# Optimization experiments

Hardware: AMD Instinct MI355X
Metric: run time of the kernel (lower is better)

Reference implementation:

```python
import jax, jax.numpy as jnp
import numpy as np

EPS_NORM = 1e-12   # torch F.normalize eps
EPS_COND = 1e-10   # conductance denominator eps (matches source)


def _metrics(rep, b):
    # rep: (N, D) float, b: (N,) int 0/1 boundaries
    N = rep.shape[0]
    S = rep @ rep.T                                   # (N, N) similarity
    # F.normalize(sim, p=2, dim=-1): L2-normalize each row
    S = S / jnp.maximum(jnp.linalg.norm(S, axis=-1, keepdims=True), EPS_NORM)
    comm = jnp.cumsum(b)                              # (N,) community ids in [0, N]
    total = S.sum()
    deg = S.sum(axis=1)                               # row sums
    # modularity: sum over same-community (i, j) of S_ij - deg_i*deg_j/total, then /total
    same = comm[:, None] == comm[None, :]
    mod = jnp.sum(jnp.where(same, S - deg[:, None] * deg[None, :] / total, 0.0)) / total
    # conductance via segment sums over community ids (num_segments fixed = N+1)
    C = N + 1
    A = jax.ops.segment_sum(S, comm, num_segments=C)          # (C, N): sum over rows i in comm c
    B2 = jax.ops.segment_sum(A.T, comm, num_segments=C)      # (C_j, C_i)
    within = jnp.diagonal(B2)                                 # within-community edge weight
    row_tot = A.sum(axis=1)                                   # total weight incident to comm c
    between = row_tot - within
    counts = jax.ops.segment_sum(jnp.ones((N,), dtype=S.dtype), comm, num_segments=C)
    nonempty = counts > 0
    cond_terms = jnp.where(nonempty, between / (2.0 * within + between + EPS_COND), 0.0)
    n_comms = jnp.maximum(nonempty.sum(), 1).astype(S.dtype)
    cond = cond_terms.sum() / n_comms
    return mod, cond


def setup_inputs() -> dict:
    key = jax.random.key(0)
    k1, k2 = jax.random.split(key)
    representations = jax.random.normal(k1, (8, 2048, 512), dtype=jnp.float32)
    boundaries = jax.random.randint(k2, (8, 2048), 0, 2, dtype=jnp.int32)
    return {"representations": representations, "boundaries": boundaries}


def reference(representations, boundaries):
    mod, cond = jax.vmap(_metrics)(representations, boundaries)
    # (2, B): row 0 = modularity per batch, row 1 = conductance per batch
    return jnp.stack([mod, cond], axis=0)
```

## Files before the change

### kernel.cpp

```cpp
#include <hip/hip_runtime.h>
#include <hip/hip_bf16.h>

constexpr int BATCH = 8;
constexpr int N = 2048;
constexpr int D = 512;

using short8 = __attribute__((ext_vector_type(8))) short;
using half8 = __attribute__((ext_vector_type(8))) _Float16;
using floatx4 = __attribute__((ext_vector_type(4))) float;

struct f8 { float4 a, b; };
__device__ __forceinline__ f8 load8(const float* p) {
    f8 r; r.a = *(const float4*)p; r.b = *(const float4*)(p + 4); return r;
}
__device__ __forceinline__ void cvt_split(const f8& v, short8& h, short8& l) {
    const float* f = (const float*)&v;
#pragma unroll
    for (int e = 0; e < 8; ++e) {
        _Float16 hh = (_Float16)f[e];
        float r = f[e] - (float)hh;
        _Float16 ll = (_Float16)r;
        h[e] = __builtin_bit_cast(short, hh);
        l[e] = __builtin_bit_cast(short, ll);
    }
}

__global__ __launch_bounds__(256) void scan_kernel(const int* __restrict__ b,
                                                   int* __restrict__ comm,
                                                   float* __restrict__ stats ) {
    int batch = blockIdx.x;
    int t = threadIdx.x;

    {
        int idx = batch * 256 + t;
#pragma unroll
        for (int u = 0; u < 24; ++u) stats[idx + u * 2048] = 0.0f;
    }

    const int* bb = b + batch * N;
    int* cc = comm + batch * N;
    int vals[8];
    int s = 0;
#pragma unroll
    for (int u = 0; u < 8; ++u) { vals[u] = bb[t * 8 + u]; s += vals[u]; }

    __shared__ int ps[256];
    ps[t] = s;
    __syncthreads();
    for (int off = 1; off < 256; off <<= 1) {
        int v = (t >= off) ? ps[t - off] : 0;
        __syncthreads();
        ps[t] += v;
        __syncthreads();
    }
    int run = (t > 0) ? ps[t - 1] : 0;
#pragma unroll
    for (int u = 0; u < 8; ++u) { run += vals[u]; cc[t * 8 + u] = run; }
}

__global__ __launch_bounds__(256) void gemm_mfma(
        const float* __restrict__ R,
        const int* __restrict__ comm,
        float* __restrict__ ssq, float* __restrict__ sm, float* __restrict__ bs) {
    int batch = blockIdx.z;

    int t = blockIdx.x;
    int bi = 0;
    while (t >= (16 - bi)) { t -= (16 - bi); ++bi; }
    int bj = bi + t;
    bool diag = (bi == bj);
    int i0 = bi * 128, j0 = bj * 128;

    __shared__ unsigned short sAhi[4096], sAlo[4096], sBhi[4096], sBlo[4096];
    __shared__ int sci[128], scj[128];

    int tid = threadIdx.x;
    const int* cm = comm + batch * N;
    if (tid < 128) { sci[tid] = cm[i0 + tid]; scj[tid] = cm[j0 + tid]; }

    const size_t bo = (size_t)batch * N * D;
    int srow = tid >> 2;
    int kg = (tid & 3) ^ ((srow >> 1) & 3);
    const float* pA0 = R + bo + (size_t)(i0 + srow) * D + kg * 8;
    const float* pA1 = pA0 + (size_t)64 * D;
    const float* pB0 = R + bo + (size_t)(j0 + srow) * D + kg * 8;
    const float* pB1 = pB0 + (size_t)64 * D;

    int lane = tid & 63;
    int wv = tid >> 6;
    int wrow = wv >> 1, wcol = wv & 1;
    int l15 = lane & 15, lhi = lane >> 4;

    int offA[4], offB[4];
#pragma unroll
    for (int m = 0; m < 4; ++m) {
        int r = wrow * 64 + m * 16 + l15;
        offA[m] = r * 64 + ((lhi ^ ((r >> 1) & 3)) << 4);
        int c = wcol * 64 + m * 16 + l15;
        offB[m] = c * 64 + ((lhi ^ ((c >> 1) & 3)) << 4);
    }

    floatx4 acc[4][4];
#pragma unroll
    for (int m = 0; m < 4; ++m)
#pragma unroll
        for (int n = 0; n < 4; ++n) acc[m][n] = (floatx4){0.f, 0.f, 0.f, 0.f};

    int wbyte = tid * 16;

    f8 rA0 = load8(pA0), rA1 = load8(pA1), rB0 = load8(pB0), rB1 = load8(pB1);

#pragma unroll 1
    for (int kt = 0; kt < 16; ++kt) {
        short8 h, l;
        cvt_split(rA0, h, l);
        *(short8*)((char*)sAhi + wbyte) = h;
        *(short8*)((char*)sAlo + wbyte) = l;
        cvt_split(rA1, h, l);
        *(short8*)((char*)sAhi + wbyte + 4096) = h;
        *(short8*)((char*)sAlo + wbyte + 4096) = l;
        cvt_split(rB0, h, l);
        *(short8*)((char*)sBhi + wbyte) = h;
        *(short8*)((char*)sBlo + wbyte) = l;
        cvt_split(rB1, h, l);
        *(short8*)((char*)sBhi + wbyte + 4096) = h;
        *(short8*)((char*)sBlo + wbyte + 4096) = l;
        __syncthreads();

        if (kt < 15) {
            int ko = (kt + 1) * 32;
            rA0 = load8(pA0 + ko);
            rA1 = load8(pA1 + ko);
            rB0 = load8(pB0 + ko);
            rB1 = load8(pB1 + ko);
        }

        half8 ah[4], al[4], bh[4], bl[4];
#pragma unroll
        for (int m = 0; m < 4; ++m) {
            ah[m] = *(const half8*)((const char*)sAhi + offA[m]);
            al[m] = *(const half8*)((const char*)sAlo + offA[m]);
            bh[m] = *(const half8*)((const char*)sBhi + offB[m]);
            bl[m] = *(const half8*)((const char*)sBlo + offB[m]);
        }
#pragma unroll
        for (int m = 0; m < 4; ++m)
#pragma unroll
            for (int n = 0; n < 4; ++n) {
                acc[m][n] = __builtin_amdgcn_mfma_f32_16x16x32_f16(ah[m], bh[n], acc[m][n], 0, 0, 0);
                acc[m][n] = __builtin_amdgcn_mfma_f32_16x16x32_f16(ah[m], bl[n], acc[m][n], 0, 0, 0);
                acc[m][n] = __builtin_amdgcn_mfma_f32_16x16x32_f16(al[m], bh[n], acc[m][n], 0, 0, 0);
            }
        __syncthreads();
    }

    float* pssq = ssq + batch * N;
    float* psm = sm + batch * N;
    float* pbs = bs + batch * N;

    int cjv[4];
#pragma unroll
    for (int n = 0; n < 4; ++n) cjv[n] = scj[wcol * 64 + n * 16 + l15];

    float cq[4] = {0.f, 0.f, 0.f, 0.f};
    float cs[4] = {0.f, 0.f, 0.f, 0.f};
    float cb[4] = {0.f, 0.f, 0.f, 0.f};

#pragma unroll
    for (int m = 0; m < 4; ++m) {
#pragma unroll
        for (int rr = 0; rr < 4; ++rr) {
            int rloc = wrow * 64 + m * 16 + lhi * 4 + rr;
            int civ = sci[rloc];
            float vq = 0.f, vs = 0.f, vb = 0.f;
#pragma unroll
            for (int n = 0; n < 4; ++n) {
                float g = acc[m][n][rr];
                float gq = g * g;
                float gb = (civ == cjv[n]) ? g : 0.f;
                vq += gq; vs += g; vb += gb;
                cq[n] += gq; cs[n] += g; cb[n] += gb;
            }
#pragma unroll
            for (int msk = 8; msk >= 1; msk >>= 1) {
                vq += __shfl_xor(vq, msk);
                vs += __shfl_xor(vs, msk);
                vb += __shfl_xor(vb, msk);
            }
            if (l15 == 0) {
                atomicAdd(&pssq[i0 + rloc], vq);
                atomicAdd(&psm[i0 + rloc], vs);
                atomicAdd(&pbs[i0 + rloc], vb);
            }
        }
    }

    if (!diag) {
#pragma unroll
        for (int n = 0; n < 4; ++n) {
            cq[n] += __shfl_xor(cq[n], 16); cq[n] += __shfl_xor(cq[n], 32);
            cs[n] += __shfl_xor(cs[n], 16); cs[n] += __shfl_xor(cs[n], 32);
            cb[n] += __shfl_xor(cb[n], 16); cb[n] += __shfl_xor(cb[n], 32);
            if (lhi == 0) {
                int col = j0 + wcol * 64 + n * 16 + l15;
                atomicAdd(&pssq[col], cq[n]);
                atomicAdd(&psm[col], cs[n]);
                atomicAdd(&pbs[col], cb[n]);
            }
        }
    }
}

__global__ __launch_bounds__(1024) void finalize(const float* __restrict__ ssq,
                                                 const float* __restrict__ sm,
                                                 const float* __restrict__ bs,
                                                 const int* __restrict__ comm,
                                                 float* __restrict__ out) {
    int batch = blockIdx.x;
    const float* pssq = ssq + batch * N;
    const float* psm = sm + batch * N;
    const float* pbs = bs + batch * N;
    const int* pcomm = comm + batch * N;
    int tid = threadIdx.x;

    __shared__ float sWc[N + 1];
    __shared__ float sTc[N + 1];
    __shared__ int sCnt[N + 1];

    for (int c = tid; c < N + 1; c += 1024) { sWc[c] = 0.0f; sTc[c] = 0.0f; sCnt[c] = 0; }
    __syncthreads();

    float totalLocal = 0.0f;
    for (int i = tid; i < N; i += 1024) {
        float r = sqrtf(pssq[i]);
        r = fmaxf(r, 1e-12f);
        float deg = psm[i] / r;
        float bn = pbs[i] / r;
        int c = pcomm[i];
        atomicAdd(&sTc[c], deg);
        atomicAdd(&sWc[c], bn);
        atomicAdd(&sCnt[c], 1);
        totalLocal += deg;
    }
    __syncthreads();

    float sumW = 0.0f, sumT2 = 0.0f, condSum = 0.0f, ncomm = 0.0f;
    for (int c = tid; c < N + 1; c += 1024) {
        if (sCnt[c] > 0) {
            float W = sWc[c];
            float T = sTc[c];
            sumW += W;
            sumT2 += T * T;
            float between = T - W;
            condSum += between / (2.0f * W + between + 1e-10f);
            ncomm += 1.0f;
        }
    }

    float vals[5] = {totalLocal, sumW, sumT2, condSum, ncomm};
#pragma unroll
    for (int v = 0; v < 5; ++v)
#pragma unroll
        for (int m = 32; m >= 1; m >>= 1) vals[v] += __shfl_xor(vals[v], m);

    __shared__ float part[5][16];
    int wid = tid >> 6;
    if ((tid & 63) == 0) {
#pragma unroll
        for (int v = 0; v < 5; ++v) part[v][wid] = vals[v];
    }
    __syncthreads();

    if (tid == 0) {
        float red[5];
#pragma unroll
        for (int v = 0; v < 5; ++v) {
            float a = 0.f;
            for (int w = 0; w < 16; ++w) a += part[v][w];
            red[v] = a;
        }
        float total = red[0];
        float mod = (red[1] - red[2] / total) / total;
        float cond = red[3] / fmaxf(red[4], 1.0f);
        out[batch] = mod;
        out[BATCH + batch] = cond;
    }
}

extern "C" void kernel_launch(void* const* d_in, const int* in_sizes, int n_in,
                              void* d_out, int out_size, void* d_ws, size_t ws_size,
                              hipStream_t stream) {
    const float* rep = (const float*)d_in[0];
    const int* bnd = (const int*)d_in[1];
    float* out = (float*)d_out;

    float* ssq = (float*)d_ws;
    float* sm = ssq + BATCH * N;
    float* bs = sm + BATCH * N;
    int* comm = (int*)(bs + BATCH * N);

    scan_kernel<<<BATCH, 256, 0, stream>>>(bnd, comm, ssq);

    dim3 grid(136, 1, BATCH);
    gemm_mfma<<<grid, 256, 0, stream>>>(rep, comm, ssq, sm, bs);

    finalize<<<BATCH, 1024, 0, stream>>>(ssq, sm, bs, comm, out);
}
```

Measured before the change: 172.0 us.

## Fuse finalize into GEMM kernel via last-block ticket per batch

Removes the separate finalize kernel launch. Each GEMM block takes a per-batch ticket with an atomic after a threadfence, and the last block to finish reduces the per-row statistics into community sums and writes modularity and conductance. The shared memory arrays are merged into one 32KB buffer that the finalize step reuses, and launch bounds now request 3 blocks per CU. The cost is a serial tail where one 256-thread block does the per-batch finalize, plus atomic loads to read the accumulated stats.

After: 265.0 us. 1.54x slower.

```diff
diff --git a/kernel.cpp b/kernel.cpp
--- a/kernel.cpp
+++ b/kernel.cpp
@@ -4,6 +4,7 @@
 constexpr int BATCH = 8;
 constexpr int N = 2048;
 constexpr int D = 512;
+constexpr int NBLK = 136;
 
 using short8 = __attribute__((ext_vector_type(8))) short;
 using half8 = __attribute__((ext_vector_type(8))) _Float16;
@@ -27,7 +28,8 @@
 
 __global__ __launch_bounds__(256) void scan_kernel(const int* __restrict__ b,
                                                    int* __restrict__ comm,
-                                                   float* __restrict__ stats ) {
+                                                   float* __restrict__ stats ,
+                                                   int* __restrict__ tickets ) {
     int batch = blockIdx.x;
     int t = threadIdx.x;
 
@@ -36,6 +38,7 @@
 #pragma unroll
         for (int u = 0; u < 24; ++u) stats[idx + u * 2048] = 0.0f;
     }
+    if (t == 0) tickets[batch] = 0;
 
     const int* bb = b + batch * N;
     int* cc = comm + batch * N;
@@ -58,21 +61,24 @@
     for (int u = 0; u < 8; ++u) { run += vals[u]; cc[t * 8 + u] = run; }
 }
 
-__global__ __launch_bounds__(256) void gemm_mfma(
+__global__ __launch_bounds__(256, 3) void gemm_mfma(
         const float* __restrict__ R,
         const int* __restrict__ comm,
-        float* __restrict__ ssq, float* __restrict__ sm, float* __restrict__ bs) {
+        float* __restrict__ ssq, float* __restrict__ sm, float* __restrict__ bs,
+        int* __restrict__ tickets,
+        float* __restrict__ out) {
     int batch = blockIdx.z;
 
-    int t = blockIdx.x;
+    int tt = blockIdx.x;
     int bi = 0;
-    while (t >= (16 - bi)) { t -= (16 - bi); ++bi; }
-    int bj = bi + t;
+    while (tt >= (16 - bi)) { tt -= (16 - bi); ++bi; }
+    int bj = bi + tt;
     bool diag = (bi == bj);
     int i0 = bi * 128, j0 = bj * 128;
 
-    __shared__ unsigned short sAhi[4096], sAlo[4096], sBhi[4096], sBlo[4096];
+    __shared__ __align__(16) unsigned char SMEM[32768];
     __shared__ int sci[128], scj[128];
+    __shared__ int sIsLast;
 
     int tid = threadIdx.x;
     const int* cm = comm + batch * N;
@@ -114,17 +120,17 @@
     for (int kt = 0; kt < 16; ++kt) {
         short8 h, l;
         cvt_split(rA0, h, l);
-        *(short8*)((char*)sAhi + wbyte) = h;
-        *(short8*)((char*)sAlo + wbyte) = l;
+        *(short8*)(SMEM + wbyte) = h;
+        *(short8*)(SMEM + 8192 + wbyte) = l;
         cvt_split(rA1, h, l);
-        *(short8*)((char*)sAhi + wbyte + 4096) = h;
-        *(short8*)((char*)sAlo + wbyte + 4096) = l;
+        *(short8*)(SMEM + 4096 + wbyte) = h;
+        *(short8*)(SMEM + 8192 + 4096 + wbyte) = l;
         cvt_split(rB0, h, l);
-        *(short8*)((char*)sBhi + wbyte) = h;
-        *(short8*)((char*)sBlo + wbyte) = l;
+        *(short8*)(SMEM + 16384 + wbyte) = h;
+        *(short8*)(SMEM + 24576 + wbyte) = l;
         cvt_split(rB1, h, l);
-        *(short8*)((char*)sBhi + wbyte + 4096) = h;
-        *(short8*)((char*)sBlo + wbyte + 4096) = l;
+        *(short8*)(SMEM + 16384 + 4096 + wbyte) = h;
+        *(short8*)(SMEM + 24576 + 4096 + wbyte) = l;
         __syncthreads();
 
         if (kt < 15) {
@@ -138,10 +144,10 @@
         half8 ah[4], al[4], bh[4], bl[4];
 #pragma unroll
         for (int m = 0; m < 4; ++m) {
-            ah[m] = *(const half8*)((const char*)sAhi + offA[m]);
-            al[m] = *(const half8*)((const char*)sAlo + offA[m]);
-            bh[m] = *(const half8*)((const char*)sBhi + offB[m]);
-            bl[m] = *(const half8*)((const char*)sBlo + offB[m]);
+            ah[m] = *(const half8*)(SMEM + offA[m]);
+            al[m] = *(const half8*)(SMEM + 8192 + offA[m]);
+            bh[m] = *(const half8*)(SMEM + 16384 + offB[m]);
+            bl[m] = *(const half8*)(SMEM + 24576 + offB[m]);
         }
 #pragma unroll
         for (int m = 0; m < 4; ++m)
@@ -209,46 +215,45 @@
             }
         }
     }
-}
-
-__global__ __launch_bounds__(1024) void finalize(const float* __restrict__ ssq,
-                                                 const float* __restrict__ sm,
-                                                 const float* __restrict__ bs,
-                                                 const int* __restrict__ comm,
-                                                 float* __restrict__ out) {
-    int batch = blockIdx.x;
-    const float* pssq = ssq + batch * N;
-    const float* psm = sm + batch * N;
-    const float* pbs = bs + batch * N;
-    const int* pcomm = comm + batch * N;
-    int tid = threadIdx.x;
-
-    __shared__ float sWc[N + 1];
-    __shared__ float sTc[N + 1];
-    __shared__ int sCnt[N + 1];
-
-    for (int c = tid; c < N + 1; c += 1024) { sWc[c] = 0.0f; sTc[c] = 0.0f; sCnt[c] = 0; }
-    __syncthreads();
-
-    float totalLocal = 0.0f;
-    for (int i = tid; i < N; i += 1024) {
-        float r = sqrtf(pssq[i]);
-        r = fmaxf(r, 1e-12f);
-        float deg = psm[i] / r;
-        float bn = pbs[i] / r;
-        int c = pcomm[i];
-        atomicAdd(&sTc[c], deg);
-        atomicAdd(&sWc[c], bn);
-        atomicAdd(&sCnt[c], 1);
+
+    __threadfence();
+    __syncthreads();
+    if (tid == 0) {
+        int old = atomicAdd(&tickets[batch], 1);
+        sIsLast = (old == NBLK - 1);
+    }
+    __syncthreads();
+    if (!sIsLast) return;
+
+    float* fWc = (float*)SMEM;
+    float* fTc = (float*)(SMEM + 2064 * 4);
+    int* fCnt = (int*)(SMEM + 4128 * 4);
+    float* red = (float*)(SMEM + 6192 * 4);
+
+    for (int c = tid; c < N + 1; c += 256) { fWc[c] = 0.f; fTc[c] = 0.f; fCnt[c] = 0; }
+    __syncthreads();
+
+    float totalLocal = 0.f;
+    for (int i = tid; i < N; i += 256) {
+        float q = atomicAdd(&pssq[i], 0.0f);
+        float s = atomicAdd(&psm[i], 0.0f);
+        float b = atomicAdd(&pbs[i], 0.0f);
+        float r = fmaxf(sqrtf(q), 1e-12f);
+        float deg = s / r;
+        float bn = b / r;
+        int c = cm[i];
+        atomicAdd(&fTc[c], deg);
+        atomicAdd(&fWc[c], bn);
+        atomicAdd(&fCnt[c], 1);
         totalLocal += deg;
     }
     __syncthreads();
 
-    float sumW = 0.0f, sumT2 = 0.0f, condSum = 0.0f, ncomm = 0.0f;
-    for (int c = tid; c < N + 1; c += 1024) {
-        if (sCnt[c] > 0) {
-            float W = sWc[c];
-            float T = sTc[c];
+    float sumW = 0.f, sumT2 = 0.f, condSum = 0.f, ncomm = 0.f;
+    for (int c = tid; c < N + 1; c += 256) {
+        if (fCnt[c] > 0) {
+            float W = fWc[c];
+            float T = fTc[c];
             sumW += W;
             sumT2 += T * T;
             float between = T - W;
@@ -261,29 +266,21 @@
 #pragma unroll
     for (int v = 0; v < 5; ++v)
 #pragma unroll
-        for (int m = 32; m >= 1; m >>= 1) vals[v] += __shfl_xor(vals[v], m);
-
-    __shared__ float part[5][16];
-    int wid = tid >> 6;
+        for (int msk = 32; msk >= 1; msk >>= 1) vals[v] += __shfl_xor(vals[v], msk);
+    __syncthreads();
     if ((tid & 63) == 0) {
 #pragma unroll
-        for (int v = 0; v < 5; ++v) part[v][wid] = vals[v];
-    }
-    __syncthreads();
-
+        for (int v = 0; v < 5; ++v) red[v * 4 + (tid >> 6)] = vals[v];
+    }
+    __syncthreads();
     if (tid == 0) {
-        float red[5];
-#pragma unroll
-        for (int v = 0; v < 5; ++v) {
-            float a = 0.f;
-            for (int w = 0; w < 16; ++w) a += part[v][w];
-            red[v] = a;
-        }
-        float total = red[0];
-        float mod = (red[1] - red[2] / total) / total;
-        float cond = red[3] / fmaxf(red[4], 1.0f);
-        out[batch] = mod;
-        out[BATCH + batch] = cond;
+        float r5[5];
+#pragma unroll
+        for (int v = 0; v < 5; ++v)
+            r5[v] = red[v * 4] + red[v * 4 + 1] + red[v * 4 + 2] + red[v * 4 + 3];
+        float total = r5[0];
+        out[batch] = (r5[1] - r5[2] / total) / total;
+        out[BATCH + batch] = r5[3] / fmaxf(r5[4], 1.0f);
     }
 }
 
@@ -298,11 +295,10 @@
     float* sm = ssq + BATCH * N;
     float* bs = sm + BATCH * N;
     int* comm = (int*)(bs + BATCH * N);
-
-    scan_kernel<<<BATCH, 256, 0, stream>>>(bnd, comm, ssq);
-
-    dim3 grid(136, 1, BATCH);
-    gemm_mfma<<<grid, 256, 0, stream>>>(rep, comm, ssq, sm, bs);
-
-    finalize<<<BATCH, 1024, 0, stream>>>(ssq, sm, bs, comm, out);
-}
+    int* tickets = comm + BATCH * N;
+
+    scan_kernel<<<BATCH, 256, 0, stream>>>(bnd, comm, ssq, tickets);
+
+    dim3 grid(NBLK, 1, BATCH);
+    gemm_mfma<<<grid, 256, 0, stream>>>(rep, comm, ssq, sm, bs, tickets, out);
+}
```
